# Kernel optimization log

Hardware: AMD Instinct MI355X
Metric: run time of the kernel (lower is better)

The kernel has to match this reference:

```python
import jax, jax.numpy as jnp
import numpy as np

FEAT = 128
N_NODES = 20000
N_EDGES = 100000
N_GRAPHS = 64


def _gcn(x, edge_index, edge_weight, W, b):
    """PyG-style GCNConv: add self loops, symmetric deg norm, scatter-add aggregate."""
    N = x.shape[0]
    row, col = edge_index[0], edge_index[1]  # source -> target
    sl = jnp.arange(N)
    row = jnp.concatenate([row, sl])
    col = jnp.concatenate([col, sl])
    ew = jnp.concatenate([edge_weight, jnp.ones((N,), x.dtype)])
    deg = jax.ops.segment_sum(ew, col, num_segments=N)
    dis = jnp.where(deg > 0, 1.0 / jnp.sqrt(deg), 0.0)
    norm = dis[row] * ew * dis[col]  # [E+N]
    h = x @ W                        # [N, out]
    out = jax.ops.segment_sum(norm[:, None] * h[row], col, num_segments=N)
    return out + b


def _pool(x, batch, num_graphs):
    ones = jnp.ones((x.shape[0],), x.dtype)
    cnt = jax.ops.segment_sum(ones, batch, num_segments=num_graphs)
    mean = jax.ops.segment_sum(x, batch, num_segments=num_graphs) / jnp.maximum(cnt, 1.0)[:, None]
    mx = jax.ops.segment_max(x, batch, num_segments=num_graphs)
    mx = jnp.where(cnt[:, None] > 0, mx, 0.0)
    return jnp.concatenate([mean, mx], axis=1)  # [G, 2F]


def setup_inputs() -> dict:
    key = jax.random.key(0)
    ks = jax.random.split(key, 24)
    F = FEAT
    d = {}
    d["x0"] = jax.random.normal(ks[0], (N_NODES, F), jnp.float32)
    d["edge_attr0"] = jax.random.uniform(ks[1], (N_EDGES, 4), jnp.float32)
    d["edge_index0"] = jax.random.randint(ks[2], (2, N_EDGES), 0, N_NODES)
    d["x1"] = jax.random.normal(ks[3], (N_NODES, F), jnp.float32)
    d["edge_attr1"] = jax.random.uniform(ks[4], (N_EDGES, 4), jnp.float32)
    d["edge_index1"] = jax.random.randint(ks[5], (2, N_EDGES), 0, N_NODES)
    d["batch0"] = jnp.sort(jax.random.randint(ks[6], (N_NODES,), 0, N_GRAPHS))
    d["batch1"] = jnp.sort(jax.random.randint(ks[7], (N_NODES,), 0, N_GRAPHS))
    s = 0.05
    d["W1A"] = jax.random.normal(ks[8], (F, F), jnp.float32) * s
    d["b1A"] = jnp.zeros((F,), jnp.float32)
    d["W1B"] = jax.random.normal(ks[9], (F, F), jnp.float32) * s
    d["b1B"] = jnp.zeros((F,), jnp.float32)
    d["W1C"] = jax.random.normal(ks[10], (F, F), jnp.float32) * s
    d["b1C"] = jnp.zeros((F,), jnp.float32)
    d["W1D"] = jax.random.normal(ks[11], (F, F), jnp.float32) * s
    d["b1D"] = jnp.zeros((F,), jnp.float32)
    d["W2"] = jax.random.normal(ks[12], (4 * F, 2 * F), jnp.float32) * s
    d["b2"] = jnp.zeros((2 * F,), jnp.float32)
    d["W3"] = jax.random.normal(ks[13], (2 * F, F), jnp.float32) * s
    d["b3"] = jnp.zeros((F,), jnp.float32)
    d["Wm1"] = jax.random.normal(ks[14], (4 * F, 8), jnp.float32) * s
    d["bm1"] = jnp.zeros((8,), jnp.float32)
    d["Wm2"] = jax.random.normal(ks[15], (8, 2), jnp.float32) * s
    d["bm2"] = jnp.zeros((2,), jnp.float32)
    return d


def _tower(x, ea, ei, batch, W1A, b1A, W1B, b1B, W1C, b1C, W1D, b1D, W2, b2, W3, b3):
    hA = jax.nn.relu(_gcn(x, ei, ea[:, 0], W1A, b1A))
    hB = jax.nn.relu(_gcn(x, ei, ea[:, 1], W1B, b1B))
    hC = jax.nn.relu(_gcn(x, ei, ea[:, 2], W1C, b1C))
    hD = jax.nn.relu(_gcn(x, ei, ea[:, 3], W1D, b1D))
    h = jnp.concatenate([hA, hB, hC, hD], axis=1)  # [N, 4F]
    ones = jnp.ones((ei.shape[1],), x.dtype)
    h = jax.nn.relu(_gcn(h, ei, ones, W2, b2))     # [N, 2F]
    h = _gcn(h, ei, ones, W3, b3)                  # [N, F]
    return _pool(h, batch, N_GRAPHS)               # [G, 2F]


def reference(x0, edge_attr0, edge_index0, x1, edge_attr1, edge_index1, batch0, batch1,
              W1A, b1A, W1B, b1B, W1C, b1C, W1D, b1D, W2, b2, W3, b3, Wm1, bm1, Wm2, bm2):
    p0 = _tower(x0, edge_attr0, edge_index0, batch0,
                W1A, b1A, W1B, b1B, W1C, b1C, W1D, b1D, W2, b2, W3, b3)
    p1 = _tower(x1, edge_attr1, edge_index1, batch1,
                W1A, b1A, W1B, b1B, W1C, b1C, W1D, b1D, W2, b2, W3, b3)
    h = jnp.concatenate([p0, p1], axis=1)  # [G, 4F]; dropout is identity in eval mode
    h = jax.nn.relu(h @ Wm1 + bm1)
    return h @ Wm2 + bm2  # [G, 2]
```

## Files before the change

kernel.cpp:

```cpp
#include <hip/hip_runtime.h>
#include <math.h>

#define NN 20000
#define EE 100000
#define GG 64
#define KP 32

typedef __attribute__((ext_vector_type(8))) short short8;
typedef __attribute__((ext_vector_type(8))) unsigned short us8;
typedef __attribute__((ext_vector_type(4))) float v4f;

__device__ __forceinline__ unsigned short f2bf(float f) {
  union { float f; unsigned u; } v;
  v.f = f;
  unsigned r = v.u + 0x7fff + ((v.u >> 16) & 1);
  return (unsigned short)(r >> 16);
}
__device__ __forceinline__ float bf2f(unsigned short s) {
  union { unsigned u; float f; } v;
  v.u = ((unsigned)s) << 16;
  return v.f;
}
__device__ __forceinline__ unsigned fenc(float x) {
  unsigned u = __float_as_uint(x);
  return (u & 0x80000000u) ? ~u : (u | 0x80000000u);
}
__device__ __forceinline__ float fdec(unsigned u) {
  unsigned b = (u & 0x80000000u) ? (u ^ 0x80000000u) : ~u;
  return __uint_as_float(b);
}

__device__ __forceinline__ void g2lds16(const unsigned short* g, unsigned short* l) {
  auto gp = reinterpret_cast<const __attribute__((address_space(1))) unsigned int*>(
      reinterpret_cast<uintptr_t>(g));
  auto lp = reinterpret_cast<__attribute__((address_space(3))) unsigned int*>(
      reinterpret_cast<uintptr_t>(l));
  __builtin_amdgcn_global_load_lds(gp, lp, 16, 0, 0);
}

__global__ void prep_kernel(const float* __restrict__ WA, const float* __restrict__ WB,
                            const float* __restrict__ WC, const float* __restrict__ WD,
                            const float* __restrict__ bA, const float* __restrict__ bB,
                            const float* __restrict__ bC, const float* __restrict__ bD,
                            const float* __restrict__ W2, const float* __restrict__ W3,
                            const float* __restrict__ x0, const float* __restrict__ x1,
                            unsigned short* __restrict__ Wt1, unsigned short* __restrict__ W2t,
                            unsigned short* __restrict__ W3t, float* __restrict__ bcat,
                            float* __restrict__ Psum, unsigned* __restrict__ Pmax,
                            int* __restrict__ cnt, unsigned short* __restrict__ xbf,
                            int N2, int xhalf) {
  int i = blockIdx.x * blockDim.x + threadIdx.x;
  if (i < xhalf) { xbf[i] = f2bf(x0[i]); return; }
  if (i < 2 * xhalf) { xbf[i] = f2bf(x1[i - xhalf]); return; }
  i -= 2 * xhalf;
  if (i < 512) {
    int X = i >> 7, j = i & 127;
    const float* b = (X == 0) ? bA : (X == 1) ? bB : (X == 2) ? bC : bD;
    bcat[i] = b[j];
  }
  if (i < 65536) {
    int col = i >> 7, k = i & 127;
    int X = col >> 7, j = col & 127;
    const float* W = (X == 0) ? WA : (X == 1) ? WB : (X == 2) ? WC : WD;
    Wt1[col * 128 + k] = f2bf(W[k * 128 + j]);
    return;
  }
  i -= 65536;
  if (i < 131072) {
    int n = i >> 9, k = i & 511;
    W2t[n * 512 + k] = f2bf(W2[(size_t)k * 256 + n]);
    return;
  }
  i -= 131072;
  if (i < 32768) {
    int n = i >> 8, k = i & 255;
    W3t[n * 256 + k] = f2bf(W3[(size_t)k * 128 + n]);
    return;
  }
  i -= 32768;
  if (i < 16384) {
    Psum[i] = 0.f;
    Pmax[i] = 0u;
    return;
  }
  i -= 16384;
  if (i < N2) cnt[i] = 0;
}

__global__ void fill_adj(const int* __restrict__ ei0, const int* __restrict__ ei1,
                         int* __restrict__ cnt, int* __restrict__ adje,
                         int* __restrict__ adjr, int E, int N) {
  int idx = blockIdx.x * blockDim.x + threadIdx.x;
  if (idx >= 2 * E) return;
  int t = idx >= E;
  int e = idx - t * E;
  const int* ei = t ? ei1 : ei0;
  int c = ei[E + e];
  int gn = t * N + c;
  int pos = atomicAdd(&cnt[gn], 1);
  if (pos < KP) {
    adje[gn * KP + pos] = idx;
    adjr[gn * KP + pos] = t * N + ei[e];
  }
}

__global__ void deg_adj(const float* __restrict__ ea0, const float* __restrict__ ea1,
                        const int* __restrict__ cnt, const int* __restrict__ adje,
                        float* __restrict__ dis, int E, int N) {
  int gn = blockIdx.x * blockDim.x + threadIdx.x;
  if (gn >= 2 * N) return;
  int t = gn >= N;
  int n = gn - t * N;
  int d = cnt[gn];
  if (d > KP) d = KP;
  float s0 = 1.f, s1 = 1.f, s2 = 1.f, s3 = 1.f;
  for (int j = 0; j < d; ++j) {
    int ge = adje[gn * KP + j];
    int e = ge - (ge >= E ? E : 0);
    const float* ea = (ge >= E) ? ea1 : ea0;
    float4 w = *(const float4*)(ea + 4 * (size_t)e);
    s0 += w.x; s1 += w.y; s2 += w.z; s3 += w.w;
  }
  float* dg = dis + (size_t)t * 5 * N;
  dg[0 * N + n] = rsqrtf(s0);
  dg[1 * N + n] = rsqrtf(s1);
  dg[2 * N + n] = rsqrtf(s2);
  dg[3 * N + n] = rsqrtf(s3);
  dg[4 * N + n] = rsqrtf(1.f + (float)d);
}

__global__ void norm_adj(const float* __restrict__ ea0, const float* __restrict__ ea1,
                         const int* __restrict__ cnt, const int* __restrict__ adje,
                         const int* __restrict__ adjr, const float* __restrict__ dis,
                         float4* __restrict__ norm4, float* __restrict__ normc,
                         int E, int N) {
  int idx = blockIdx.x * blockDim.x + threadIdx.x;
  if (idx >= 2 * N * KP) return;
  int gn = idx >> 5, j = idx & (KP - 1);
  int d = cnt[gn];
  if (j >= d || j >= KP) return;
  int t = gn >= N;
  int c = gn - t * N;
  int ge = adje[idx];
  int e = ge - t * E;
  const float* ea = t ? ea1 : ea0;
  const float* dg = dis + (size_t)t * 5 * N;
  int r = adjr[idx] - t * N;
  float4 w = *(const float4*)(ea + 4 * (size_t)e);
  float4 o;
  o.x = dg[0 * N + r] * w.x * dg[0 * N + c];
  o.y = dg[1 * N + r] * w.y * dg[1 * N + c];
  o.z = dg[2 * N + r] * w.z * dg[2 * N + c];
  o.w = dg[3 * N + r] * w.w * dg[3 * N + c];
  norm4[idx] = o;
  normc[idx] = dg[4 * N + r] * dg[4 * N + c];
}

__global__ __launch_bounds__(128) void gather4(const unsigned short* __restrict__ X,
                                               const int* __restrict__ adjr,
                                               const int* __restrict__ cnt,
                                               const float4* __restrict__ norm4,
                                               const float* __restrict__ dis,
                                               unsigned short* __restrict__ Y, int N) {
  int tid = threadIdx.x;
  int gn = blockIdx.x * 8 + (tid >> 4);
  if (gn >= 2 * N) return;
  int t = gn >= N;
  int n = gn - t * N;
  int fq = (tid & 15) << 3;
  const float* dg = dis + (size_t)t * 5 * N;
  us8 xs = *(const us8*)(X + (size_t)gn * 128 + fq);
  float xf[8];
#pragma unroll
  for (int j = 0; j < 8; ++j) xf[j] = bf2f(xs[j]);
  float acc[4][8];
#pragma unroll
  for (int p = 0; p < 4; ++p) {
    float d = dg[p * N + n];
    float dd = d * d;
#pragma unroll
    for (int j = 0; j < 8; ++j) acc[p][j] = dd * xf[j];
  }
  int deg = cnt[gn];
  if (deg > KP) deg = KP;
  int base = gn * KP;
  int i = 0;
  for (; i + 3 < deg; i += 4) {
    int r0 = adjr[base + i], r1 = adjr[base + i + 1];
    int r2 = adjr[base + i + 2], r3 = adjr[base + i + 3];
    float4 w0 = norm4[base + i], w1 = norm4[base + i + 1];
    float4 w2 = norm4[base + i + 2], w3 = norm4[base + i + 3];
    us8 h0 = *(const us8*)(X + (size_t)r0 * 128 + fq);
    us8 h1 = *(const us8*)(X + (size_t)r1 * 128 + fq);
    us8 h2 = *(const us8*)(X + (size_t)r2 * 128 + fq);
    us8 h3 = *(const us8*)(X + (size_t)r3 * 128 + fq);
#pragma unroll
    for (int j = 0; j < 8; ++j) {
      float f0 = bf2f(h0[j]), f1 = bf2f(h1[j]);
      float f2 = bf2f(h2[j]), f3 = bf2f(h3[j]);
      acc[0][j] += w0.x * f0 + w1.x * f1 + w2.x * f2 + w3.x * f3;
      acc[1][j] += w0.y * f0 + w1.y * f1 + w2.y * f2 + w3.y * f3;
      acc[2][j] += w0.z * f0 + w1.z * f1 + w2.z * f2 + w3.z * f3;
      acc[3][j] += w0.w * f0 + w1.w * f1 + w2.w * f2 + w3.w * f3;
    }
  }
  for (; i < deg; ++i) {
    int r = adjr[base + i];
    float4 w = norm4[base + i];
    us8 hr = *(const us8*)(X + (size_t)r * 128 + fq);
#pragma unroll
    for (int j = 0; j < 8; ++j) {
      float h = bf2f(hr[j]);
      acc[0][j] += w.x * h;
      acc[1][j] += w.y * h;
      acc[2][j] += w.z * h;
      acc[3][j] += w.w * h;
    }
  }
#pragma unroll
  for (int p = 0; p < 4; ++p) {
    us8 o;
#pragma unroll
    for (int j = 0; j < 8; ++j) o[j] = f2bf(acc[p][j]);
    *(us8*)(Y + (size_t)gn * 512 + p * 128 + fq) = o;
  }
}

__global__ __launch_bounds__(256) void gemm_diag(const unsigned short* __restrict__ A,
                                                 const unsigned short* __restrict__ Wt1,
                                                 const float* __restrict__ bias,
                                                 unsigned short* __restrict__ Cb, int M) {
  __shared__ unsigned short As[128 * 64];
  __shared__ unsigned short Bs[128 * 64];
  int tid = threadIdx.x;
  int wave = tid >> 6, lane = tid & 63;
  int quad = lane >> 4, l16 = lane & 15;
  int n0 = blockIdx.x * 128;
  int m0 = blockIdx.y * 128;
  int wm = (wave >> 1) * 64, wn = (wave & 1) * 64;
  v4f acc[4][4] = {};
  for (int k0 = 0; k0 < 128; k0 += 64) {
#pragma unroll
    for (int l = 0; l < 4; ++l) {
      int idx = tid + (l << 8);
      int row = idx >> 3, seg = idx & 7;
      int gm = m0 + row;
      if (gm >= M) gm = M - 1;
      g2lds16(A + (size_t)gm * 512 + n0 + k0 + (seg << 3), As + idx * 8);
      int gb = n0 + row;
      g2lds16(Wt1 + (size_t)gb * 128 + k0 + (seg << 3), Bs + idx * 8);
    }
    __syncthreads();
#pragma unroll
    for (int kk = 0; kk < 2; ++kk) {
      short8 af[4], bfr[4];
#pragma unroll
      for (int r = 0; r < 4; ++r)
        af[r] = *(const short8*)(As + (wm + r * 16 + l16) * 64 + kk * 32 + quad * 8);
#pragma unroll
      for (int c = 0; c < 4; ++c)
        bfr[c] = *(const short8*)(Bs + (wn + c * 16 + l16) * 64 + kk * 32 + quad * 8);
#pragma unroll
      for (int r = 0; r < 4; ++r)
#pragma unroll
        for (int c = 0; c < 4; ++c)
          acc[r][c] = __builtin_amdgcn_mfma_f32_16x16x32_bf16(af[r], bfr[c], acc[r][c], 0, 0, 0);
    }
    __syncthreads();
  }
#pragma unroll
  for (int r = 0; r < 4; ++r) {
    int row_base = m0 + wm + r * 16 + quad * 4;
#pragma unroll
    for (int j = 0; j < 4; ++j) {
      int gm = row_base + j;
      if (gm >= M) continue;
#pragma unroll
      for (int c = 0; c < 4; ++c) {
        int col = n0 + wn + c * 16 + l16;
        float v = acc[r][c][j] + bias[col];
        Cb[(size_t)gm * 512 + col] = f2bf(fmaxf(v, 0.f));
      }
    }
  }
}

__global__ __launch_bounds__(256) void gemm_mfma(const unsigned short* __restrict__ A,
                                                 const unsigned short* __restrict__ Bt,
                                                 unsigned short* __restrict__ Cb,
                                                 int M, int N, int K) {
  __shared__ unsigned short As[128 * 64];
  __shared__ unsigned short Bs[128 * 64];
  int tid = threadIdx.x;
  int wave = tid >> 6, lane = tid & 63;
  int quad = lane >> 4, l16 = lane & 15;
  int m0 = blockIdx.y * 128, n0 = blockIdx.x * 128;
  int wm = (wave >> 1) * 64, wn = (wave & 1) * 64;
  v4f acc[4][4] = {};
  for (int k0 = 0; k0 < K; k0 += 64) {
#pragma unroll
    for (int l = 0; l < 4; ++l) {
      int idx = tid + (l << 8);
      int row = idx >> 3, seg = idx & 7;
      int gm = m0 + row;
      if (gm >= M) gm = M - 1;
      g2lds16(A + (size_t)gm * K + k0 + (seg << 3), As + idx * 8);
      int gn = n0 + row;
      g2lds16(Bt + (size_t)gn * K + k0 + (seg << 3), Bs + idx * 8);
    }
    __syncthreads();
#pragma unroll
    for (int kk = 0; kk < 2; ++kk) {
      short8 af[4], bfr[4];
#pragma unroll
      for (int r = 0; r < 4; ++r)
        af[r] = *(const short8*)(As + (wm + r * 16 + l16) * 64 + kk * 32 + quad * 8);
#pragma unroll
      for (int c = 0; c < 4; ++c)
        bfr[c] = *(const short8*)(Bs + (wn + c * 16 + l16) * 64 + kk * 32 + quad * 8);
#pragma unroll
      for (int r = 0; r < 4; ++r)
#pragma unroll
        for (int c = 0; c < 4; ++c)
          acc[r][c] = __builtin_amdgcn_mfma_f32_16x16x32_bf16(af[r], bfr[c], acc[r][c], 0, 0, 0);
    }
    __syncthreads();
  }
#pragma unroll
  for (int r = 0; r < 4; ++r) {
    int row_base = m0 + wm + r * 16 + quad * 4;
#pragma unroll
    for (int j = 0; j < 4; ++j) {
      int gm = row_base + j;
      if (gm >= M) continue;
      unsigned short* cp = Cb + (size_t)gm * N + n0 + wn;
#pragma unroll
      for (int c = 0; c < 4; ++c) cp[c * 16 + l16] = f2bf(acc[r][c][j]);
    }
  }
}

__global__ __launch_bounds__(128) void agg_gather_b(const unsigned short* __restrict__ H,
                                                    const int* __restrict__ adjr,
                                                    const int* __restrict__ cnt,
                                                    const float* __restrict__ normc,
                                                    const float* __restrict__ dis,
                                                    const float* __restrict__ bias,
                                                    unsigned short* __restrict__ OutB,
                                                    int N, int F) {
  int per8 = F >> 3;
  int tid = threadIdx.x;
  int gn = blockIdx.x * (128 / per8) + tid / per8;
  if (gn >= 2 * N) return;
  int t = gn >= N;
  int n = gn - t * N;
  int fq = (tid % per8) << 3;
  float d = dis[(size_t)(t * 5 + 4) * N + n];
  float dd = d * d;
  us8 hs = *(const us8*)(H + (size_t)gn * F + fq);
  float acc[8];
#pragma unroll
  for (int i = 0; i < 8; ++i) acc[i] = dd * bf2f(hs[i]) + bias[fq + i];
  int deg = cnt[gn];
  if (deg > KP) deg = KP;
  int base = gn * KP;
  int i = 0;
  for (; i + 3 < deg; i += 4) {
    int r0 = adjr[base + i], r1 = adjr[base + i + 1];
    int r2 = adjr[base + i + 2], r3 = adjr[base + i + 3];
    float n0 = normc[base + i], n1 = normc[base + i + 1];
    float n2 = normc[base + i + 2], n3 = normc[base + i + 3];
    us8 h0 = *(const us8*)(H + (size_t)r0 * F + fq);
    us8 h1 = *(const us8*)(H + (size_t)r1 * F + fq);
    us8 h2 = *(const us8*)(H + (size_t)r2 * F + fq);
    us8 h3 = *(const us8*)(H + (size_t)r3 * F + fq);
#pragma unroll
    for (int j = 0; j < 8; ++j)
      acc[j] += n0 * bf2f(h0[j]) + n1 * bf2f(h1[j]) + n2 * bf2f(h2[j]) + n3 * bf2f(h3[j]);
  }
  for (; i < deg; ++i) {
    int r = adjr[base + i];
    float nv = normc[base + i];
    us8 hr = *(const us8*)(H + (size_t)r * F + fq);
#pragma unroll
    for (int j = 0; j < 8; ++j) acc[j] += nv * bf2f(hr[j]);
  }
  us8 o;
#pragma unroll
  for (int i2 = 0; i2 < 8; ++i2) o[i2] = f2bf(fmaxf(acc[i2], 0.f));
  *(us8*)(OutB + (size_t)gn * F + fq) = o;
}

__global__ __launch_bounds__(256) void agg3_pool(const unsigned short* __restrict__ H,
                                                 const int* __restrict__ adjr,
                                                 const int* __restrict__ cnt,
                                                 const float* __restrict__ normc,
                                                 const float* __restrict__ dis,
                                                 const float* __restrict__ bias,
                                                 const int* __restrict__ batch0,
                                                 const int* __restrict__ batch1,
                                                 float* __restrict__ Psum,
                                                 unsigned* __restrict__ Pmax, int N) {
  __shared__ float sS[16 * 128];
  __shared__ int bg[16];
  int tid = threadIdx.x;
  int nl = tid >> 4;
  int gn = blockIdx.x * 16 + nl;
  int fq = (tid & 15) << 3;
  if (tid < 16) {
    int g2 = blockIdx.x * 16 + tid;
    bg[tid] = (g2 < N) ? batch0[g2] : 64 + batch1[g2 - N];
  }
  int t = gn >= N;
  int n = gn - t * N;
  float d = dis[(size_t)(t * 5 + 4) * N + n];
  float dd = d * d;
  us8 hs = *(const us8*)(H + (size_t)gn * 128 + fq);
  float acc[8];
#pragma unroll
  for (int i = 0; i < 8; ++i) acc[i] = dd * bf2f(hs[i]) + bias[fq + i];
  int deg = cnt[gn];
  if (deg > KP) deg = KP;
  int base = gn * KP;
  int i = 0;
  for (; i + 3 < deg; i += 4) {
    int r0 = adjr[base + i], r1 = adjr[base + i + 1];
    int r2 = adjr[base + i + 2], r3 = adjr[base + i + 3];
    float n0 = normc[base + i], n1 = normc[base + i + 1];
    float n2 = normc[base + i + 2], n3 = normc[base + i + 3];
    us8 h0 = *(const us8*)(H + (size_t)r0 * 128 + fq);
    us8 h1 = *(const us8*)(H + (size_t)r1 * 128 + fq);
    us8 h2 = *(const us8*)(H + (size_t)r2 * 128 + fq);
    us8 h3 = *(const us8*)(H + (size_t)r3 * 128 + fq);
#pragma unroll
    for (int j = 0; j < 8; ++j)
      acc[j] += n0 * bf2f(h0[j]) + n1 * bf2f(h1[j]) + n2 * bf2f(h2[j]) + n3 * bf2f(h3[j]);
  }
  for (; i < deg; ++i) {
    int r = adjr[base + i];
    float nv = normc[base + i];
    us8 hr = *(const us8*)(H + (size_t)r * 128 + fq);
#pragma unroll
    for (int j = 0; j < 8; ++j) acc[j] += nv * bf2f(hr[j]);
  }
#pragma unroll
  for (int j = 0; j < 8; ++j) sS[nl * 128 + fq + j] = acc[j];
  __syncthreads();
  int f = tid;
  if (f >= 128) return;
  int cur = bg[0];
  float sum = 0.f, mx = -3.4e38f;
  for (int k = 0; k < 16; ++k) {
    int g = bg[k];
    if (g != cur) {
      atomicAdd(&Psum[cur * 128 + f], sum);
      atomicMax(&Pmax[cur * 128 + f], fenc(mx));
      sum = 0.f;
      mx = -3.4e38f;
      cur = g;
    }
    float v = sS[k * 128 + f];
    sum += v;
    mx = fmaxf(mx, v);
  }
  atomicAdd(&Psum[cur * 128 + f], sum);
  atomicMax(&Pmax[cur * 128 + f], fenc(mx));
}

__device__ __forceinline__ int lower_bound_i(const int* a, int n, int key) {
  int lo = 0, hi = n;
  while (lo < hi) {
    int mid = (lo + hi) >> 1;
    if (a[mid] < key) lo = mid + 1; else hi = mid;
  }
  return lo;
}

__global__ __launch_bounds__(128) void poolmlp_kernel(const int* __restrict__ batch0,
                                                      const int* __restrict__ batch1,
                                                      const float* __restrict__ Psum,
                                                      const unsigned* __restrict__ Pmax,
                                                      const float* __restrict__ Wm1,
                                                      const float* __restrict__ bm1,
                                                      const float* __restrict__ Wm2,
                                                      const float* __restrict__ bm2,
                                                      float* __restrict__ out, int N) {
  __shared__ float sP[512];
  __shared__ float h8[8];
  int g = blockIdx.x;
  int f = threadIdx.x;
  {
    int s = lower_bound_i(batch0, N, g);
    int e = lower_bound_i(batch0, N, g + 1);
    int cnt = e - s;
    sP[f] = (cnt > 0) ? Psum[g * 128 + f] / (float)cnt : 0.f;
    sP[128 + f] = (cnt > 0) ? fdec(Pmax[g * 128 + f]) : 0.f;
  }
  {
    int s = lower_bound_i(batch1, N, g);
    int e = lower_bound_i(batch1, N, g + 1);
    int cnt = e - s;
    sP[256 + f] = (cnt > 0) ? Psum[(64 + g) * 128 + f] / (float)cnt : 0.f;
    sP[384 + f] = (cnt > 0) ? fdec(Pmax[(64 + g) * 128 + f]) : 0.f;
  }
  __syncthreads();
  if (f < 8) {
    float s = bm1[f];
    for (int k = 0; k < 512; ++k) s += sP[k] * Wm1[k * 8 + f];
    h8[f] = fmaxf(s, 0.f);
  }
  __syncthreads();
  if (f < 2) {
    float s = bm2[f];
#pragma unroll
    for (int t = 0; t < 8; ++t) s += h8[t] * Wm2[t * 2 + f];
    out[g * 2 + f] = s;
  }
}

extern "C" void kernel_launch(void* const* d_in, const int* in_sizes, int n_in,
                              void* d_out, int out_size, void* d_ws, size_t ws_size,
                              hipStream_t stream) {
  const int N = NN, E = EE;
  const int N2 = 2 * N, E2 = 2 * E;
  float* ws = (float*)d_ws;

  size_t o_bcat = 0;
  size_t o_dis = o_bcat + 512;
  size_t o_Psum = o_dis + 10 * (size_t)N;
  size_t o_Pmax = o_Psum + 128 * 128;
  size_t o_n4 = ((o_Pmax + 128 * 128) + 3) & ~(size_t)3;
  size_t o_nc = o_n4 + 4 * (size_t)N2 * KP;
  size_t o_int = o_nc + (size_t)N2 * KP;
  size_t int_count = (size_t)N2 + 2 * (size_t)N2 * KP;
  size_t o_bf = (o_int + int_count + 7) & ~(size_t)7;

  float* bcat = ws + o_bcat;
  float* dis = ws + o_dis;
  float* Psum = ws + o_Psum;
  unsigned* Pmax = (unsigned*)(ws + o_Pmax);
  float4* norm4 = (float4*)(ws + o_n4);
  float* normc = ws + o_nc;
  int* cnt = (int*)(ws + o_int);
  int* adje = cnt + N2;
  int* adjr = adje + (size_t)N2 * KP;
  unsigned short* bfb = (unsigned short*)(ws + o_bf);
  unsigned short* Wt1 = bfb;
  unsigned short* W2t = Wt1 + 512 * 128;
  unsigned short* W3t = W2t + 256 * 512;
  unsigned short* xbf = W3t + 128 * 256;
  unsigned short* Ybf = xbf + (size_t)N2 * 128;
  unsigned short* Gbf = Ybf + (size_t)N2 * 512;
  unsigned short* Hbf = Gbf + (size_t)N2 * 512;

  const float* b2 = (const float*)d_in[17];
  const float* b3 = (const float*)d_in[19];
  const float* ea0 = (const float*)d_in[1];
  const int* ei0 = (const int*)d_in[2];
  const float* ea1 = (const float*)d_in[4];
  const int* ei1 = (const int*)d_in[5];
  const int* batch0 = (const int*)d_in[6];
  const int* batch1 = (const int*)d_in[7];

  {
    int xhalf = N * 128;
    int total = 2 * xhalf + 65536 + 131072 + 32768 + 16384 + N2;
    prep_kernel<<<(total + 255) / 256, 256, 0, stream>>>(
        (const float*)d_in[8], (const float*)d_in[10], (const float*)d_in[12],
        (const float*)d_in[14], (const float*)d_in[9], (const float*)d_in[11],
        (const float*)d_in[13], (const float*)d_in[15], (const float*)d_in[16],
        (const float*)d_in[18], (const float*)d_in[0], (const float*)d_in[3],
        Wt1, W2t, W3t, bcat, Psum, Pmax, cnt, xbf, N2, xhalf);
  }

  fill_adj<<<(E2 + 255) / 256, 256, 0, stream>>>(ei0, ei1, cnt, adje, adjr, E, N);
  deg_adj<<<(N2 + 255) / 256, 256, 0, stream>>>(ea0, ea1, cnt, adje, dis, E, N);
  norm_adj<<<(N2 * KP + 255) / 256, 256, 0, stream>>>(ea0, ea1, cnt, adje, adjr, dis,
                                                      norm4, normc, E, N);

  gather4<<<(N2 + 7) / 8, 128, 0, stream>>>(xbf, adjr, cnt, norm4, dis, Ybf, N);
  {
    dim3 grid(4, (N2 + 127) / 128);
    gemm_diag<<<grid, 256, 0, stream>>>(Ybf, Wt1, bcat, Gbf, N2);
  }
  {
    dim3 grid(2, (N2 + 127) / 128);
    gemm_mfma<<<grid, 256, 0, stream>>>(Gbf, W2t, Hbf, N2, 256, 512);
    agg_gather_b<<<(N2 + 3) / 4, 128, 0, stream>>>(Hbf, adjr, cnt, normc, dis, b2, Gbf, N, 256);
  }
  {
    dim3 grid(1, (N2 + 127) / 128);
    gemm_mfma<<<grid, 256, 0, stream>>>(Gbf, W3t, Hbf, N2, 128, 256);
    agg3_pool<<<N2 / 16, 256, 0, stream>>>(Hbf, adjr, cnt, normc, dis, b3, batch0, batch1,
                                           Psum, Pmax, N);
  }
  poolmlp_kernel<<<GG, 128, 0, stream>>>(batch0, batch1, Psum, Pmax, (const float*)d_in[20],
                                         (const float*)d_in[21], (const float*)d_in[22],
                                         (const float*)d_in[23], (float*)d_out, N);
}
```

Before: 288.8 us.

## Pack edge attributes into adjacency slots and widen layer-2 GEMM tile

fill_adj now copies each edge's float4 attribute straight into a per-node adjacency slot array (eaP), replacing the edge-id array (adje). deg_adj and norm_adj then read attributes contiguously instead of through an indirect random gather. Separately, the layer-2 GEMM gets a dedicated kernel with 128x256 tiles that cover the full output width per block, so each A tile is loaded once instead of twice. The cost is more workspace for eaP, a larger shared-memory footprint and more accumulator registers in gemm_l2, which may lower occupancy, plus half as many GEMM blocks.

```diff
diff --git a/kernel.cpp b/kernel.cpp
--- a/kernel.cpp
+++ b/kernel.cpp
@@ -88,25 +88,26 @@
 }
 
 __global__ void fill_adj(const int* __restrict__ ei0, const int* __restrict__ ei1,
-                         int* __restrict__ cnt, int* __restrict__ adje,
-                         int* __restrict__ adjr, int E, int N) {
+                         const float* __restrict__ ea0, const float* __restrict__ ea1,
+                         int* __restrict__ cnt, int* __restrict__ adjr,
+                         float4* __restrict__ eaP, int E, int N) {
   int idx = blockIdx.x * blockDim.x + threadIdx.x;
   if (idx >= 2 * E) return;
   int t = idx >= E;
   int e = idx - t * E;
   const int* ei = t ? ei1 : ei0;
+  const float* ea = t ? ea1 : ea0;
   int c = ei[E + e];
   int gn = t * N + c;
   int pos = atomicAdd(&cnt[gn], 1);
   if (pos < KP) {
-    adje[gn * KP + pos] = idx;
     adjr[gn * KP + pos] = t * N + ei[e];
-  }
-}
-
-__global__ void deg_adj(const float* __restrict__ ea0, const float* __restrict__ ea1,
-                        const int* __restrict__ cnt, const int* __restrict__ adje,
-                        float* __restrict__ dis, int E, int N) {
+    eaP[gn * KP + pos] = *(const float4*)(ea + 4 * (size_t)e);
+  }
+}
+
+__global__ void deg_adj(const float4* __restrict__ eaP, const int* __restrict__ cnt,
+                        float* __restrict__ dis, int N) {
   int gn = blockIdx.x * blockDim.x + threadIdx.x;
   if (gn >= 2 * N) return;
   int t = gn >= N;
@@ -115,10 +116,7 @@
   if (d > KP) d = KP;
   float s0 = 1.f, s1 = 1.f, s2 = 1.f, s3 = 1.f;
   for (int j = 0; j < d; ++j) {
-    int ge = adje[gn * KP + j];
-    int e = ge - (ge >= E ? E : 0);
-    const float* ea = (ge >= E) ? ea1 : ea0;
-    float4 w = *(const float4*)(ea + 4 * (size_t)e);
+    float4 w = eaP[gn * KP + j];
     s0 += w.x; s1 += w.y; s2 += w.z; s3 += w.w;
   }
   float* dg = dis + (size_t)t * 5 * N;
@@ -129,11 +127,9 @@
   dg[4 * N + n] = rsqrtf(1.f + (float)d);
 }
 
-__global__ void norm_adj(const float* __restrict__ ea0, const float* __restrict__ ea1,
-                         const int* __restrict__ cnt, const int* __restrict__ adje,
+__global__ void norm_adj(const float4* __restrict__ eaP, const int* __restrict__ cnt,
                          const int* __restrict__ adjr, const float* __restrict__ dis,
-                         float4* __restrict__ norm4, float* __restrict__ normc,
-                         int E, int N) {
+                         float4* __restrict__ norm4, float* __restrict__ normc, int N) {
   int idx = blockIdx.x * blockDim.x + threadIdx.x;
   if (idx >= 2 * N * KP) return;
   int gn = idx >> 5, j = idx & (KP - 1);
@@ -141,12 +137,9 @@
   if (j >= d || j >= KP) return;
   int t = gn >= N;
   int c = gn - t * N;
-  int ge = adje[idx];
-  int e = ge - t * E;
-  const float* ea = t ? ea1 : ea0;
   const float* dg = dis + (size_t)t * 5 * N;
   int r = adjr[idx] - t * N;
-  float4 w = *(const float4*)(ea + 4 * (size_t)e);
+  float4 w = eaP[idx];
   float4 o;
   o.x = dg[0 * N + r] * w.x * dg[0 * N + c];
   o.y = dg[1 * N + r] * w.y * dg[1 * N + c];
@@ -281,6 +274,65 @@
         float v = acc[r][c][j] + bias[col];
         Cb[(size_t)gm * 512 + col] = f2bf(fmaxf(v, 0.f));
       }
+    }
+  }
+}
+
+__global__ __launch_bounds__(256) void gemm_l2(const unsigned short* __restrict__ A,
+                                               const unsigned short* __restrict__ Bt,
+                                               unsigned short* __restrict__ Cb, int M) {
+  __shared__ unsigned short As[128 * 64];
+  __shared__ unsigned short Bs[256 * 64];
+  const int K = 512, Nc = 256;
+  int tid = threadIdx.x;
+  int wave = tid >> 6, lane = tid & 63;
+  int quad = lane >> 4, l16 = lane & 15;
+  int m0 = blockIdx.x * 128;
+  int wm = (wave >> 1) * 64, wn = (wave & 1) * 128;
+  v4f acc[4][8] = {};
+  for (int k0 = 0; k0 < K; k0 += 64) {
+#pragma unroll
+    for (int l = 0; l < 4; ++l) {
+      int idx = tid + (l << 8);
+      int row = idx >> 3, seg = idx & 7;
+      int gm = m0 + row;
+      if (gm >= M) gm = M - 1;
+      g2lds16(A + (size_t)gm * K + k0 + (seg << 3), As + idx * 8);
+    }
+#pragma unroll
+    for (int l = 0; l < 8; ++l) {
+      int idx = tid + (l << 8);
+      int row = idx >> 3, seg = idx & 7;
+      g2lds16(Bt + (size_t)row * K + k0 + (seg << 3), Bs + idx * 8);
+    }
+    __syncthreads();
+#pragma unroll
+    for (int kk = 0; kk < 2; ++kk) {
+      short8 af[4], bfr[8];
+#pragma unroll
+      for (int r = 0; r < 4; ++r)
+        af[r] = *(const short8*)(As + (wm + r * 16 + l16) * 64 + kk * 32 + quad * 8);
+#pragma unroll
+      for (int c = 0; c < 8; ++c)
+        bfr[c] = *(const short8*)(Bs + (wn + c * 16 + l16) * 64 + kk * 32 + quad * 8);
+#pragma unroll
+      for (int r = 0; r < 4; ++r)
+#pragma unroll
+        for (int c = 0; c < 8; ++c)
+          acc[r][c] = __builtin_amdgcn_mfma_f32_16x16x32_bf16(af[r], bfr[c], acc[r][c], 0, 0, 0);
+    }
+    __syncthreads();
+  }
+#pragma unroll
+  for (int r = 0; r < 4; ++r) {
+    int row_base = m0 + wm + r * 16 + quad * 4;
+#pragma unroll
+    for (int j = 0; j < 4; ++j) {
+      int gm = row_base + j;
+      if (gm >= M) continue;
+      unsigned short* cp = Cb + (size_t)gm * Nc + wn;
+#pragma unroll
+      for (int c = 0; c < 8; ++c) cp[c * 16 + l16] = f2bf(acc[r][c][j]);
     }
   }
 }
@@ -530,9 +582,10 @@
   size_t o_Psum = o_dis + 10 * (size_t)N;
   size_t o_Pmax = o_Psum + 128 * 128;
   size_t o_n4 = ((o_Pmax + 128 * 128) + 3) & ~(size_t)3;
-  size_t o_nc = o_n4 + 4 * (size_t)N2 * KP;
+  size_t o_ea = o_n4 + 4 * (size_t)N2 * KP;
+  size_t o_nc = o_ea + 4 * (size_t)N2 * KP;
   size_t o_int = o_nc + (size_t)N2 * KP;
-  size_t int_count = (size_t)N2 + 2 * (size_t)N2 * KP;
+  size_t int_count = (size_t)N2 + (size_t)N2 * KP;
   size_t o_bf = (o_int + int_count + 7) & ~(size_t)7;
 
   float* bcat = ws + o_bcat;
@@ -540,10 +593,10 @@
   float* Psum = ws + o_Psum;
   unsigned* Pmax = (unsigned*)(ws + o_Pmax);
   float4* norm4 = (float4*)(ws + o_n4);
+  float4* eaP = (float4*)(ws + o_ea);
   float* normc = ws + o_nc;
   int* cnt = (int*)(ws + o_int);
-  int* adje = cnt + N2;
-  int* adjr = adje + (size_t)N2 * KP;
+  int* adjr = cnt + N2;
   unsigned short* bfb = (unsigned short*)(ws + o_bf);
   unsigned short* Wt1 = bfb;
   unsigned short* W2t = Wt1 + 512 * 128;
@@ -573,21 +626,17 @@
         Wt1, W2t, W3t, bcat, Psum, Pmax, cnt, xbf, N2, xhalf);
   }
 
-  fill_adj<<<(E2 + 255) / 256, 256, 0, stream>>>(ei0, ei1, cnt, adje, adjr, E, N);
-  deg_adj<<<(N2 + 255) / 256, 256, 0, stream>>>(ea0, ea1, cnt, adje, dis, E, N);
-  norm_adj<<<(N2 * KP + 255) / 256, 256, 0, stream>>>(ea0, ea1, cnt, adje, adjr, dis,
-                                                      norm4, normc, E, N);
+  fill_adj<<<(E2 + 255) / 256, 256, 0, stream>>>(ei0, ei1, ea0, ea1, cnt, adjr, eaP, E, N);
+  deg_adj<<<(N2 + 255) / 256, 256, 0, stream>>>(eaP, cnt, dis, N);
+  norm_adj<<<(N2 * KP + 255) / 256, 256, 0, stream>>>(eaP, cnt, adjr, dis, norm4, normc, N);
 
   gather4<<<(N2 + 7) / 8, 128, 0, stream>>>(xbf, adjr, cnt, norm4, dis, Ybf, N);
   {
     dim3 grid(4, (N2 + 127) / 128);
     gemm_diag<<<grid, 256, 0, stream>>>(Ybf, Wt1, bcat, Gbf, N2);
   }
-  {
-    dim3 grid(2, (N2 + 127) / 128);
-    gemm_mfma<<<grid, 256, 0, stream>>>(Gbf, W2t, Hbf, N2, 256, 512);
-    agg_gather_b<<<(N2 + 3) / 4, 128, 0, stream>>>(Hbf, adjr, cnt, normc, dis, b2, Gbf, N, 256);
-  }
+  gemm_l2<<<(N2 + 127) / 128, 256, 0, stream>>>(Gbf, W2t, Hbf, N2);
+  agg_gather_b<<<(N2 + 3) / 4, 128, 0, stream>>>(Hbf, adjr, cnt, normc, dis, b2, Gbf, N, 256);
   {
     dim3 grid(1, (N2 + 127) / 128);
     gemm_mfma<<<grid, 256, 0, stream>>>(Gbf, W3t, Hbf, N2, 128, 256);
```

Result: no change. 293.7 us (+1.7%).
